# Optimization experiments

Measured on AMD Instinct MI355X. Metric: run time of the kernel, lower is better.

Reference implementation:

```python
import jax, jax.numpy as jnp
import numpy as np

EPS_PD = 1e-6    # torch F.pairwise_distance eps (added to x - y before norm)
EPS_NORM = 1e-12  # torch F.normalize eps


def l2_normalize(x):
    n = jnp.sqrt(jnp.sum(x * x, axis=1, keepdims=True))
    return x / jnp.maximum(n, EPS_NORM)


def pairwise_l2(x, y):
    # Faithful to ||x_i - y_j + eps||_2 (torch pairwise_distance adds scalar eps
    # to every coordinate of the difference) but computed via Gram matrices
    D = x.shape[1]
    xx = jnp.sum(x * x, axis=1)            # [B]
    yy = jnp.sum(y * y, axis=1)            # [B]
    xy = x @ y.T                           # [B, B]
    sq = xx[:, None] + yy[None, :] - 2.0 * xy
    # cross terms from the +eps shift: 2*eps*sum(x_i - y_j) + D*eps^2
    sq = sq + 2.0 * EPS_PD * (jnp.sum(x, axis=1)[:, None] - jnp.sum(y, axis=1)[None, :])
    sq = sq + D * (EPS_PD * EPS_PD)
    return jnp.sqrt(jnp.maximum(sq, 0.0))


def setup_inputs() -> dict:
    key = jax.random.key(0)
    k1, k2 = jax.random.split(key)
    B, D = 4096, 512
    low_feature = jax.random.normal(k1, (B, D), dtype=jnp.float32)
    embed_feature = jax.random.normal(k2, (B, D), dtype=jnp.float32)
    id_numpy = jnp.arange(B, dtype=jnp.int64 if jax.config.read('jax_enable_x64') else jnp.int32).reshape(B, 1)
    return {"low_feature": low_feature, "embed_feature": embed_feature, "id_numpy": id_numpy}


def reference(low_feature, embed_feature, id_numpy):
    # ids are unique (arange), so the set()-dedup in the original is identity.
    B = low_feature.shape[0]
    K = B  # k_num == current_batch_size -> x_start = y_start = 0

    low_n = l2_normalize(low_feature)
    emb_n = l2_normalize(embed_feature)

    dist_low = pairwise_l2(low_n, low_n)      # [B, B]
    dist_embed = pairwise_l2(emb_n, emb_n)    # [B, B]

    dl1 = dist_low[: K - 1, : K - 2]
    dl2 = dist_low[: K - 1, 1 : K - 1]
    de1 = dist_embed[: K - 1, : K - 2]
    de2 = dist_embed[: K - 1, 1 : K - 1]

    coeff = jnp.sign(dl1 - dl2) - jnp.sign(de1 - de2)
    dist_embed_inverse = de2 - de1
    loss_structure = jnp.mean(coeff * dist_embed_inverse)
    return loss_structure
```

## Files before the change

### kernel.cpp

```cpp
#include <hip/hip_runtime.h>
#include <hip/hip_bf16.h>
#include <hip/hip_fp8.h>
#include <math.h>

#define BROWS 4096
#define DIM   512
#define YEMB_B 2097152
#define TSTRIDE 191
#define NT 22

typedef float f32x4 __attribute__((ext_vector_type(4)));

__global__ __launch_bounds__(256) void prep4_kernel(
    const float* __restrict__ low, const float* __restrict__ emb,
    unsigned char* __restrict__ Yq,
    float* __restrict__ s_l, float* __restrict__ r_l,
    float* __restrict__ s_e, float* __restrict__ r_e,
    float* __restrict__ out) {
  const int tid = threadIdx.x;
  const int lane = tid & 63, wid = tid >> 6;
  const int rid = blockIdx.x * 4 + wid;
  if (blockIdx.x == 0 && tid == 0) out[0] = 0.f;

  const bool is_low = (rid < BROWS);
  const int row = is_low ? rid : rid - BROWS;
  const float* x = (is_low ? low : emb) + (size_t)row * DIM;

  const float4 v0 = ((const float4*)x)[lane * 2];
  const float4 v1 = ((const float4*)x)[lane * 2 + 1];

  float ss = v0.x * v0.x + v0.y * v0.y + v0.z * v0.z + v0.w * v0.w +
             v1.x * v1.x + v1.y * v1.y + v1.z * v1.z + v1.w * v1.w;
#pragma unroll
  for (int o = 1; o < 64; o <<= 1) ss += __shfl_xor(ss, o, 64);
  const float inv = 1.0f / fmaxf(sqrtf(ss), 1e-12f);

  float y[8] = {v0.x * inv, v0.y * inv, v0.z * inv, v0.w * inv,
                v1.x * inv, v1.y * inv, v1.z * inv, v1.w * inv};

  union { unsigned char b[8]; unsigned long long u; } pk;
  float sv = 0.f, rv = 0.f;
#pragma unroll
  for (int i = 0; i < 8; ++i) {
    pk.b[i] = __hip_fp8_e4m3(y[i]).__x;
    sv += y[i] * y[i];
    rv += y[i];
  }
  ((unsigned long long*)(Yq + (size_t)rid * 512))[lane] = pk.u;

#pragma unroll
  for (int o = 1; o < 64; o <<= 1) {
    sv += __shfl_xor(sv, o, 64);
    rv += __shfl_xor(rv, o, 64);
  }
  if (lane == 0) {
    (is_low ? s_l : s_e)[row] = sv;
    (is_low ? r_l : r_e)[row] = rv;
  }
}

__global__ __launch_bounds__(512, 2) void fused_sym_kernel(
    const unsigned char* __restrict__ Yq,
    const float* __restrict__ s_l, const float* __restrict__ r_l,
    const float* __restrict__ s_e, const float* __restrict__ r_e,
    float* __restrict__ out) {
  __shared__ __align__(16) unsigned char lds8[98304];
  __shared__ float hand_d[4][48][2];
  __shared__ float hand_t[4][192][2];
  __shared__ float sred[8];

  int rem = blockIdx.x, br = 0;
  while (rem >= NT - br) { rem -= NT - br; ++br; }
  const int bc = br + rem;
  const bool diag = (br == bc);

  const int tid = threadIdx.x;
  const int lane = tid & 63;
  const int wid = tid >> 6;
  const int wr = wid >> 1;
  const int wc = wid & 1;
  const int quad = lane >> 4, cpos = lane & 15;
  const int r0 = br * TSTRIDE, c0 = bc * TSTRIDE;

  int goff[6];
#pragma unroll
  for (int s = 0; s < 6; ++s) {
    const int c = tid + 512 * s;
    const int seg = c / 768;
    const int within = c - seg * 768;
    const int rp = within >> 3;
    const int cc = within & 7;
    const int rloc = 2 * rp + (cc >> 2);
    const int gch = (cc & 3) ^ (rp & 3);
    int base;
    if (seg == 0)      base = min(r0 + rloc, BROWS - 1) * 512;
    else if (seg == 1) base = YEMB_B + min(r0 + rloc, BROWS - 1) * 512;
    else if (seg == 2) base = min(c0 + rloc, BROWS - 1) * 512;
    else               base = YEMB_B + min(c0 + rloc, BROWS - 1) * 512;
    goff[s] = base + (gch << 4);
  }

  auto STAGE = [&](int t, int b) {
    const int k0 = t * 64;
#pragma unroll
    for (int s = 0; s < 6; ++s) {
      if (s < 3 || !diag)
        __builtin_amdgcn_global_load_lds(
            (const __attribute__((address_space(1))) void*)(Yq + goff[s] + k0),
            (__attribute__((address_space(3))) void*)(lds8 + b * 49152 +
                                                      (tid + 512 * s) * 16),
            16, 0, 0);
    }
  };

  const int RaH = (48 * wr + cpos) >> 1;
  const int s3a = RaH & 3;
  const int aoff = RaH * 128 + (cpos & 1) * 64 + (quad & 1) * 8;
  const int RbH = (96 * wc + cpos) >> 1;
  const int s3b = RbH & 3;
  const int boff = RbH * 128 + (cpos & 1) * 64 + (quad & 1) * 8;
  const int segAL = 0, segAE = 12288;
  const int segBL = diag ? 0 : 24576;
  const int segBE = diag ? 12288 : 36864;

  f32x4 accl[3][6], acce[3][6];
#pragma unroll
  for (int u = 0; u < 3; ++u)
#pragma unroll
    for (int v = 0; v < 6; ++v) {
      accl[u][v] = (f32x4)(0.f);
      acce[u][v] = (f32x4)(0.f);
    }

  STAGE(0, 0);

  for (int t = 0; t < 8; ++t) {
    if (t < 7) STAGE(t + 1, (t + 1) & 1);
    if (t == 7)      asm volatile("s_waitcnt vmcnt(0)" ::: "memory");
    else if (diag)   asm volatile("s_waitcnt vmcnt(3)" ::: "memory");
    else             asm volatile("s_waitcnt vmcnt(6)" ::: "memory");
    __builtin_amdgcn_s_barrier();
    __builtin_amdgcn_sched_barrier(0);

    const unsigned char* Lb = lds8 + (t & 1) * 49152;
#pragma unroll
    for (int kk = 0; kk < 2; ++kk) {
      const int q = 2 * kk + (quad >> 1);
      const int cha = aoff + ((q ^ s3a) << 4);
      const int chb = boff + ((q ^ s3b) << 4);
      {
        long a[3], b[6];
#pragma unroll
        for (int u = 0; u < 3; ++u) a[u] = *(const long*)(Lb + segAL + cha + u * 1024);
#pragma unroll
        for (int v = 0; v < 6; ++v) b[v] = *(const long*)(Lb + segBL + chb + v * 1024);
        __builtin_amdgcn_s_setprio(1);
#pragma unroll
        for (int u = 0; u < 3; ++u)
#pragma unroll
          for (int v = 0; v < 6; ++v)
            accl[u][v] = __builtin_amdgcn_mfma_f32_16x16x32_fp8_fp8(
                a[u], b[v], accl[u][v], 0, 0, 0);
        __builtin_amdgcn_s_setprio(0);
      }
      {
        long a[3], b[6];
#pragma unroll
        for (int u = 0; u < 3; ++u) a[u] = *(const long*)(Lb + segAE + cha + u * 1024);
#pragma unroll
        for (int v = 0; v < 6; ++v) b[v] = *(const long*)(Lb + segBE + chb + v * 1024);
        __builtin_amdgcn_s_setprio(1);
#pragma unroll
        for (int u = 0; u < 3; ++u)
#pragma unroll
          for (int v = 0; v < 6; ++v)
            acce[u][v] = __builtin_amdgcn_mfma_f32_16x16x32_fp8_fp8(
                a[u], b[v], acce[u][v], 0, 0, 0);
        __builtin_amdgcn_s_setprio(0);
      }
    }
    __builtin_amdgcn_sched_barrier(0);
    __builtin_amdgcn_s_barrier();
    __builtin_amdgcn_sched_barrier(0);
  }

  const float epst = (float)DIM * 1e-6f * 1e-6f;
#pragma unroll
  for (int v = 0; v < 6; ++v) {
    const int j = min(c0 + 96 * wc + 16 * v + cpos, BROWS - 1);
    const float sjl = s_l[j], rjl = r_l[j];
    const float sje = s_e[j], rje = r_e[j];
#pragma unroll
    for (int u = 0; u < 3; ++u)
#pragma unroll
      for (int r = 0; r < 4; ++r) {
        const int i = min(r0 + 48 * wr + 16 * u + 4 * quad + r, BROWS - 1);
        const float sql = s_l[i] + sjl - 2.f * accl[u][v][r] +
                          2e-6f * (r_l[i] - rjl) + epst;
        accl[u][v][r] = sqrtf(fmaxf(sql, 0.f));
        const float sqe = s_e[i] + sje - 2.f * acce[u][v][r] +
                          2e-6f * (r_e[i] - rje) + epst;
        acce[u][v][r] = sqrtf(fmaxf(sqe, 0.f));
      }
  }

  if (wc == 1 && cpos == 0) {
#pragma unroll
    for (int u = 0; u < 3; ++u)
#pragma unroll
      for (int r = 0; r < 4; ++r) {
        hand_d[wr][16 * u + 4 * quad + r][0] = accl[u][0][r];
        hand_d[wr][16 * u + 4 * quad + r][1] = acce[u][0][r];
      }
  }
  if (quad == 0 && wr >= 1) {
#pragma unroll
    for (int v = 0; v < 6; ++v) {
      hand_t[wr - 1][96 * wc + 16 * v + cpos][0] = accl[0][v][0];
      hand_t[wr - 1][96 * wc + 16 * v + cpos][1] = acce[0][v][0];
    }
  }
  __syncthreads();

  float sum = 0.f;

  const int srcin = (lane & 48) | ((cpos + 1) & 15);
#pragma unroll
  for (int u = 0; u < 3; ++u)
#pragma unroll
    for (int r = 0; r < 4; ++r) {
      const int trow = 48 * wr + 16 * u + 4 * quad + r;
      const int i = r0 + trow;
      const bool rowok = (trow <= TSTRIDE - 1) && (i <= BROWS - 2);
#pragma unroll
      for (int v = 0; v < 6; ++v) {
        const float dl1 = accl[u][v][r], de1 = acce[u][v][r];
        float dl2 = __shfl(dl1, srcin, 64);
        float de2 = __shfl(de1, srcin, 64);
        if (v < 5) {
          const float dlb = __shfl(accl[u][v + 1][r], lane & 48, 64);
          const float deb = __shfl(acce[u][v + 1][r], lane & 48, 64);
          if (cpos == 15) { dl2 = dlb; de2 = deb; }
        } else if (cpos == 15 && wc == 0) {
          dl2 = hand_d[wr][16 * u + 4 * quad + r][0];
          de2 = hand_d[wr][16 * u + 4 * quad + r][1];
        }
        const int tcol = 96 * wc + 16 * v + cpos;
        const int j = c0 + tcol;
        if (rowok && tcol <= TSTRIDE - 1 && j <= BROWS - 3) {
          const float aa = dl1 - dl2, bb = de1 - de2;
          const float coeff = (float)((aa > 0.f) - (aa < 0.f)) -
                              (float)((bb > 0.f) - (bb < 0.f));
          sum += coeff * (de2 - de1);
        }
      }
    }

  if (!diag) {
#pragma unroll
    for (int u = 0; u < 3; ++u)
#pragma unroll
      for (int v = 0; v < 6; ++v) {
        const int tcol = 96 * wc + 16 * v + cpos;
        const int ii = c0 + tcol;
        const bool colok = (tcol <= TSTRIDE - 1) && (ii <= BROWS - 2);
#pragma unroll
        for (int r = 0; r < 4; ++r) {
          const int trow = 48 * wr + 16 * u + 4 * quad + r;
          const int jj = r0 + trow;
          float dl2, de2;
          if (r < 3) {
            dl2 = accl[u][v][r + 1];
            de2 = acce[u][v][r + 1];
          } else {
            const float dlq = __shfl(accl[u][v][0], (lane + 16) & 63, 64);
            const float deq = __shfl(acce[u][v][0], (lane + 16) & 63, 64);
            const int un = (u < 2) ? u + 1 : u;
            const float dlu = __shfl(accl[un][v][0], cpos, 64);
            const float deu = __shfl(acce[un][v][0], cpos, 64);
            if (quad < 3)    { dl2 = dlq; de2 = deq; }
            else if (u < 2)  { dl2 = dlu; de2 = deu; }
            else             { dl2 = hand_t[wr][tcol][0];
                               de2 = hand_t[wr][tcol][1]; }
          }
          if (colok && trow <= TSTRIDE - 1 && jj <= BROWS - 3) {
            const float dl1 = accl[u][v][r], de1 = acce[u][v][r];
            const float aa = dl1 - dl2, bb = de1 - de2;
            const float coeff = (float)((aa > 0.f) - (aa < 0.f)) -
                                (float)((bb > 0.f) - (bb < 0.f));
            sum += coeff * (de2 - de1);
          }
        }
      }
  }

#pragma unroll
  for (int o = 32; o; o >>= 1) sum += __shfl_down(sum, o, 64);
  if (lane == 0) sred[wid] = sum;
  __syncthreads();
  if (tid == 0) {
    const float scale = 1.0f / ((float)(BROWS - 1) * (float)(BROWS - 2));
    float t = 0.f;
#pragma unroll
    for (int w = 0; w < 8; ++w) t += sred[w];
    atomicAdd(out, t * scale);
  }
}

extern "C" void kernel_launch(void* const* d_in, const int* in_sizes, int n_in,
                              void* d_out, int out_size, void* d_ws,
                              size_t ws_size, hipStream_t stream) {
  const float* low = (const float*)d_in[0];
  const float* emb = (const float*)d_in[1];
  float* out = (float*)d_out;

  unsigned char* Yq = (unsigned char*)d_ws;
  float* s_l = (float*)(Yq + 2 * (size_t)BROWS * DIM);
  float* r_l = s_l + BROWS;
  float* r_e_dummy = nullptr; (void)r_e_dummy;
  float* s_e = r_l + BROWS;
  float* r_e = s_e + BROWS;

  prep4_kernel<<<2 * BROWS / 4, 256, 0, stream>>>(low, emb, Yq, s_l, r_l, s_e, r_e, out);
  fused_sym_kernel<<<NT * (NT + 1) / 2, 512, 0, stream>>>(Yq, s_l, r_l, s_e, r_e, out);
}
```

Measured before the change: 108.5 us.

## Split each triangular tile into two column halves per 256-thread block

Each upper-triangular 191x191 tile is split into two column halves handled by separate 4-wave blocks, which doubles the grid and shrinks LDS per block. The diagonal special case that reused the A tile as the B tile is removed, so diagonal tiles now load B separately. The first half gets a seventh 16-column MFMA group so its last column can supply the neighbour value that the hand_d exchange used to carry. This is meant to improve occupancy and load balance across CUs, at the cost of reloading A rows twice per tile and some redundant boundary compute.

```diff
diff --git a/kernel.cpp b/kernel.cpp
--- a/kernel.cpp
+++ b/kernel.cpp
@@ -59,56 +59,61 @@
   }
 }
 
-__global__ __launch_bounds__(512, 2) void fused_sym_kernel(
+__global__ __launch_bounds__(256, 2) void fused_sym_kernel(
     const unsigned char* __restrict__ Yq,
     const float* __restrict__ s_l, const float* __restrict__ r_l,
     const float* __restrict__ s_e, const float* __restrict__ r_e,
     float* __restrict__ out) {
-  __shared__ __align__(16) unsigned char lds8[98304];
-  __shared__ float hand_d[4][48][2];
-  __shared__ float hand_t[4][192][2];
-  __shared__ float sred[8];
-
-  int rem = blockIdx.x, br = 0;
+  __shared__ __align__(16) long lds_l[9728];
+  __shared__ float hand_t[3][96][2];
+  __shared__ float sred[4];
+
+  const int tri = blockIdx.x >> 1;
+  const int half = blockIdx.x & 1;
+  int rem = tri, br = 0;
   while (rem >= NT - br) { rem -= NT - br; ++br; }
   const int bc = br + rem;
   const bool diag = (br == bc);
+  const bool hasv6 = (half == 0);
 
   const int tid = threadIdx.x;
   const int lane = tid & 63;
   const int wid = tid >> 6;
-  const int wr = wid >> 1;
-  const int wc = wid & 1;
+  const int wr = wid;
   const int quad = lane >> 4, cpos = lane & 15;
-  const int r0 = br * TSTRIDE, c0 = bc * TSTRIDE;
-
-  int goff[6];
-#pragma unroll
-  for (int s = 0; s < 6; ++s) {
-    const int c = tid + 512 * s;
-    const int seg = c / 768;
-    const int within = c - seg * 768;
-    const int rp = within >> 3;
-    const int cc = within & 7;
-    const int rloc = 2 * rp + (cc >> 2);
-    const int gch = (cc & 3) ^ (rp & 3);
+  const int r0 = br * TSTRIDE;
+  const int cB = bc * TSTRIDE + half * 96;
+  const int tcbase = half * 96;
+
+  int goff[10];
+#pragma unroll
+  for (int s = 0; s < 10; ++s) {
+    const int c = tid + 256 * s;
+    const int rp = c >> 3, cc = c & 7;
+    int seg, rpl;
+    if (rp < 96)       { seg = 0; rpl = rp;       }
+    else if (rp < 192) { seg = 1; rpl = rp - 96;  }
+    else if (rp < 248) { seg = 2; rpl = rp - 192; }
+    else               { seg = 3; rpl = rp - 248; }
+    const int rloc = 2 * rpl + (cc >> 2);
+    const int gch = (cc & 3) ^ (rpl & 3);
     int base;
     if (seg == 0)      base = min(r0 + rloc, BROWS - 1) * 512;
     else if (seg == 1) base = YEMB_B + min(r0 + rloc, BROWS - 1) * 512;
-    else if (seg == 2) base = min(c0 + rloc, BROWS - 1) * 512;
-    else               base = YEMB_B + min(c0 + rloc, BROWS - 1) * 512;
+    else if (seg == 2) base = min(cB + rloc, BROWS - 1) * 512;
+    else               base = YEMB_B + min(cB + rloc, BROWS - 1) * 512;
     goff[s] = base + (gch << 4);
   }
 
   auto STAGE = [&](int t, int b) {
     const int k0 = t * 64;
 #pragma unroll
-    for (int s = 0; s < 6; ++s) {
-      if (s < 3 || !diag)
+    for (int s = 0; s < 10; ++s) {
+      if (s < 9 || tid < 128)
         __builtin_amdgcn_global_load_lds(
             (const __attribute__((address_space(1))) void*)(Yq + goff[s] + k0),
-            (__attribute__((address_space(3))) void*)(lds8 + b * 49152 +
-                                                      (tid + 512 * s) * 16),
+            (__attribute__((address_space(3))) void*)(
+                ((char*)lds_l) + b * 38912 + (tid + 256 * s) * 16),
             16, 0, 0);
     }
   };
@@ -116,18 +121,18 @@
   const int RaH = (48 * wr + cpos) >> 1;
   const int s3a = RaH & 3;
   const int aoff = RaH * 128 + (cpos & 1) * 64 + (quad & 1) * 8;
-  const int RbH = (96 * wc + cpos) >> 1;
-  const int s3b = RbH & 3;
-  const int boff = RbH * 128 + (cpos & 1) * 64 + (quad & 1) * 8;
-  const int segAL = 0, segAE = 12288;
-  const int segBL = diag ? 0 : 24576;
-  const int segBE = diag ? 12288 : 36864;
-
-  f32x4 accl[3][6], acce[3][6];
+  const int s3b = (cpos >> 1) & 3;
+  const int boff = (cpos >> 1) * 128 + (cpos & 1) * 64 + (quad & 1) * 8;
+  const int iaL = aoff >> 3;
+  const int iaE = (12288 + aoff) >> 3;
+  const int ibL = (24576 + boff) >> 3;
+  const int ibE = (31744 + boff) >> 3;
+
+  f32x4 accl[3][7], acce[3][7];
 #pragma unroll
   for (int u = 0; u < 3; ++u)
 #pragma unroll
-    for (int v = 0; v < 6; ++v) {
+    for (int v = 0; v < 7; ++v) {
       accl[u][v] = (f32x4)(0.f);
       acce[u][v] = (f32x4)(0.f);
     }
@@ -137,23 +142,24 @@
   for (int t = 0; t < 8; ++t) {
     if (t < 7) STAGE(t + 1, (t + 1) & 1);
     if (t == 7)      asm volatile("s_waitcnt vmcnt(0)" ::: "memory");
-    else if (diag)   asm volatile("s_waitcnt vmcnt(3)" ::: "memory");
-    else             asm volatile("s_waitcnt vmcnt(6)" ::: "memory");
+    else if (wid < 2) asm volatile("s_waitcnt vmcnt(10)" ::: "memory");
+    else             asm volatile("s_waitcnt vmcnt(9)" ::: "memory");
     __builtin_amdgcn_s_barrier();
     __builtin_amdgcn_sched_barrier(0);
 
-    const unsigned char* Lb = lds8 + (t & 1) * 49152;
+    const int bo = (t & 1) * 4864;
 #pragma unroll
     for (int kk = 0; kk < 2; ++kk) {
       const int q = 2 * kk + (quad >> 1);
-      const int cha = aoff + ((q ^ s3a) << 4);
-      const int chb = boff + ((q ^ s3b) << 4);
+      const int qa2 = ((q ^ s3a) << 1);
+      const int qb2 = ((q ^ s3b) << 1);
       {
-        long a[3], b[6];
-#pragma unroll
-        for (int u = 0; u < 3; ++u) a[u] = *(const long*)(Lb + segAL + cha + u * 1024);
-#pragma unroll
-        for (int v = 0; v < 6; ++v) b[v] = *(const long*)(Lb + segBL + chb + v * 1024);
+        long a[3], b[7];
+#pragma unroll
+        for (int u = 0; u < 3; ++u) a[u] = lds_l[bo + iaL + qa2 + u * 128];
+#pragma unroll
+        for (int v = 0; v < 6; ++v) b[v] = lds_l[bo + ibL + qb2 + v * 128];
+        if (hasv6) b[6] = lds_l[bo + ibL + qb2 + 768];
         __builtin_amdgcn_s_setprio(1);
 #pragma unroll
         for (int u = 0; u < 3; ++u)
@@ -161,14 +167,21 @@
           for (int v = 0; v < 6; ++v)
             accl[u][v] = __builtin_amdgcn_mfma_f32_16x16x32_fp8_fp8(
                 a[u], b[v], accl[u][v], 0, 0, 0);
+        if (hasv6) {
+#pragma unroll
+          for (int u = 0; u < 3; ++u)
+            accl[u][6] = __builtin_amdgcn_mfma_f32_16x16x32_fp8_fp8(
+                a[u], b[6], accl[u][6], 0, 0, 0);
+        }
         __builtin_amdgcn_s_setprio(0);
       }
       {
-        long a[3], b[6];
-#pragma unroll
-        for (int u = 0; u < 3; ++u) a[u] = *(const long*)(Lb + segAE + cha + u * 1024);
-#pragma unroll
-        for (int v = 0; v < 6; ++v) b[v] = *(const long*)(Lb + segBE + chb + v * 1024);
+        long a[3], b[7];
+#pragma unroll
+        for (int u = 0; u < 3; ++u) a[u] = lds_l[bo + iaE + qa2 + u * 128];
+#pragma unroll
+        for (int v = 0; v < 6; ++v) b[v] = lds_l[bo + ibE + qb2 + v * 128];
+        if (hasv6) b[6] = lds_l[bo + ibE + qb2 + 768];
         __builtin_amdgcn_s_setprio(1);
 #pragma unroll
         for (int u = 0; u < 3; ++u)
@@ -176,6 +189,12 @@
           for (int v = 0; v < 6; ++v)
             acce[u][v] = __builtin_amdgcn_mfma_f32_16x16x32_fp8_fp8(
                 a[u], b[v], acce[u][v], 0, 0, 0);
+        if (hasv6) {
+#pragma unroll
+          for (int u = 0; u < 3; ++u)
+            acce[u][6] = __builtin_amdgcn_mfma_f32_16x16x32_fp8_fp8(
+                a[u], b[6], acce[u][6], 0, 0, 0);
+        }
         __builtin_amdgcn_s_setprio(0);
       }
     }
@@ -186,8 +205,8 @@
 
   const float epst = (float)DIM * 1e-6f * 1e-6f;
 #pragma unroll
-  for (int v = 0; v < 6; ++v) {
-    const int j = min(c0 + 96 * wc + 16 * v + cpos, BROWS - 1);
+  for (int v = 0; v < 7; ++v) {
+    const int j = min(cB + 16 * v + cpos, BROWS - 1);
     const float sjl = s_l[j], rjl = r_l[j];
     const float sje = s_e[j], rje = r_e[j];
 #pragma unroll
@@ -204,20 +223,11 @@
       }
   }
 
-  if (wc == 1 && cpos == 0) {
-#pragma unroll
-    for (int u = 0; u < 3; ++u)
-#pragma unroll
-      for (int r = 0; r < 4; ++r) {
-        hand_d[wr][16 * u + 4 * quad + r][0] = accl[u][0][r];
-        hand_d[wr][16 * u + 4 * quad + r][1] = acce[u][0][r];
-      }
-  }
   if (quad == 0 && wr >= 1) {
 #pragma unroll
     for (int v = 0; v < 6; ++v) {
-      hand_t[wr - 1][96 * wc + 16 * v + cpos][0] = accl[0][v][0];
-      hand_t[wr - 1][96 * wc + 16 * v + cpos][1] = acce[0][v][0];
+      hand_t[wr - 1][16 * v + cpos][0] = accl[0][v][0];
+      hand_t[wr - 1][16 * v + cpos][1] = acce[0][v][0];
     }
   }
   __syncthreads();
@@ -237,17 +247,12 @@
         const float dl1 = accl[u][v][r], de1 = acce[u][v][r];
         float dl2 = __shfl(dl1, srcin, 64);
         float de2 = __shfl(de1, srcin, 64);
-        if (v < 5) {
-          const float dlb = __shfl(accl[u][v + 1][r], lane & 48, 64);
-          const float deb = __shfl(acce[u][v + 1][r], lane & 48, 64);
-          if (cpos == 15) { dl2 = dlb; de2 = deb; }
-        } else if (cpos == 15 && wc == 0) {
-          dl2 = hand_d[wr][16 * u + 4 * quad + r][0];
-          de2 = hand_d[wr][16 * u + 4 * quad + r][1];
-        }
-        const int tcol = 96 * wc + 16 * v + cpos;
-        const int j = c0 + tcol;
-        if (rowok && tcol <= TSTRIDE - 1 && j <= BROWS - 3) {
+        const float dlb = __shfl(accl[u][v + 1][r], lane & 48, 64);
+        const float deb = __shfl(acce[u][v + 1][r], lane & 48, 64);
+        if (cpos == 15) { dl2 = dlb; de2 = deb; }
+        const int tc = tcbase + 16 * v + cpos;
+        const int j = cB + 16 * v + cpos;
+        if (rowok && tc <= TSTRIDE - 1 && j <= BROWS - 3) {
           const float aa = dl1 - dl2, bb = de1 - de2;
           const float coeff = (float)((aa > 0.f) - (aa < 0.f)) -
                               (float)((bb > 0.f) - (bb < 0.f));
@@ -261,9 +266,9 @@
     for (int u = 0; u < 3; ++u)
 #pragma unroll
       for (int v = 0; v < 6; ++v) {
-        const int tcol = 96 * wc + 16 * v + cpos;
-        const int ii = c0 + tcol;
-        const bool colok = (tcol <= TSTRIDE - 1) && (ii <= BROWS - 2);
+        const int tc = tcbase + 16 * v + cpos;
+        const int ii = cB + 16 * v + cpos;
+        const bool colok = (tc <= TSTRIDE - 1) && (ii <= BROWS - 2);
 #pragma unroll
         for (int r = 0; r < 4; ++r) {
           const int trow = 48 * wr + 16 * u + 4 * quad + r;
@@ -280,8 +285,8 @@
             const float deu = __shfl(acce[un][v][0], cpos, 64);
             if (quad < 3)    { dl2 = dlq; de2 = deq; }
             else if (u < 2)  { dl2 = dlu; de2 = deu; }
-            else             { dl2 = hand_t[wr][tcol][0];
-                               de2 = hand_t[wr][tcol][1]; }
+            else             { dl2 = hand_t[wr][16 * v + cpos][0];
+                               de2 = hand_t[wr][16 * v + cpos][1]; }
           }
           if (colok && trow <= TSTRIDE - 1 && jj <= BROWS - 3) {
             const float dl1 = accl[u][v][r], de1 = acce[u][v][r];
@@ -302,7 +307,7 @@
     const float scale = 1.0f / ((float)(BROWS - 1) * (float)(BROWS - 2));
     float t = 0.f;
 #pragma unroll
-    for (int w = 0; w < 8; ++w) t += sred[w];
+    for (int w = 0; w < 4; ++w) t += sred[w];
     atomicAdd(out, t * scale);
   }
 }
@@ -317,10 +322,9 @@
   unsigned char* Yq = (unsigned char*)d_ws;
   float* s_l = (float*)(Yq + 2 * (size_t)BROWS * DIM);
   float* r_l = s_l + BROWS;
-  float* r_e_dummy = nullptr; (void)r_e_dummy;
   float* s_e = r_l + BROWS;
   float* r_e = s_e + BROWS;
 
   prep4_kernel<<<2 * BROWS / 4, 256, 0, stream>>>(low, emb, Yq, s_l, r_l, s_e, r_e, out);
-  fused_sym_kernel<<<NT * (NT + 1) / 2, 512, 0, stream>>>(Yq, s_l, r_l, s_e, r_e, out);
+  fused_sym_kernel<<<NT * (NT + 1), 256, 0, stream>>>(Yq, s_l, r_l, s_e, r_e, out);
 }
```

Result: no change. 110.5 us (+1.9%).
